# Optimization experiments

Hardware: AMD Instinct MI355X
Metric: run time of the kernel (lower is better)

## Reference

```python
import jax, jax.numpy as jnp
import numpy as np

N = 32768      # nodes
E = 262144     # edges
CS, CV = 32, 16      # node scalar / vector channels (32x0e + 16x1o)
MS, MV = 16, 8       # msg irreps scalar / vector channels
H = 4                # heads
NB = 16              # rbf basis
OS, OV = CS + CV, CS + CV + CV   # CG-coupler output: 48x0e + 64x1o
WNUM = CS + CS + CV + CV + CV    # 112 tensor-product path weights
SPLITS = [CS, CS + CS, CS + CS + CV, CS + CS + CV + CV]
SQRT3, SQRT2 = 3.0 ** 0.5, 2.0 ** 0.5


def _split(x, cs):
    # flat irreps vector -> (scalars [*,cs], vectors [*,cv,3])
    return x[:, :cs], x[:, cs:].reshape(x.shape[0], -1, 3)


def _lin(s, v, Ws, Wv):
    # equivariant o3.Linear: independent mixing of scalar / vector multiplicities
    return s @ Ws, jnp.einsum('ecx,cd->edx', v, Wv)


def _o3_layernorm(s, v, eps=1e-5):
    s = (s - s.mean(-1, keepdims=True)) / jnp.sqrt(s.var(-1, keepdims=True) + eps)
    n2 = jnp.mean(jnp.sum(v * v, -1), -1, keepdims=True)
    return s, v / jnp.sqrt(n2 + eps)[..., None]


def _cg(s, v, y0, y1, w_ss, w_sv, w_vs, w_vd, w_vc):
    # Clebsch-Gordan coupler for l<=1: all allowed paths, per-edge path weights
    dot = jnp.einsum('ecx,ex->ec', v, y1) / SQRT3           # 1o x 1o -> 0e
    cross = jnp.cross(v, y1[:, None, :]) / SQRT2            # 1o x 1o -> 1o
    out_s = jnp.concatenate([w_ss * s * y0[:, None], w_vd * dot], axis=-1)
    out_v = jnp.concatenate([
        w_sv[..., None] * s[..., None] * y1[:, None, :],    # 0e x 1o -> 1o
        w_vs[..., None] * v * y0[:, None, None],            # 1o x 0e -> 1o
        w_vc[..., None] * cross], axis=1)
    return out_s, out_v


def setup_inputs() -> dict:
    key = jax.random.key(0)
    ks = jax.random.split(key, 20)
    w = lambda k, shape, fan: (jax.random.normal(k, shape, jnp.float32) / np.sqrt(fan).astype(np.float32))
    return {
        'node': jax.random.normal(ks[0], (N, CS + 3 * CV), jnp.float32),
        'rbf': jax.random.uniform(ks[1], (E, NB), jnp.float32),
        'rsh': jax.random.normal(ks[2], (E, 4), jnp.float32),
        'Wsrc_s': w(ks[3], (CS, CS), CS), 'Wsrc_v': w(ks[4], (CV, CV), CV),
        'Wdst_s': w(ks[5], (CS, CS), CS), 'Wdst_v': w(ks[6], (CV, CV), CV),
        'W_rbf': w(ks[7], (NB, WNUM), NB),
        'dtp2_w': jax.random.normal(ks[8], (WNUM,), jnp.float32),
        'Wa': w(ks[9], (OS, MS * H), OS),
        'alpha_dot': w(ks[10], (1, H, MS), MS),
        'Wval_s': w(ks[11], (OS, CS), OS), 'Wval_v': w(ks[12], (OV, CV), OV),
        'Wg': w(ks[13], (CS, CV), CS),
        'Wvl_s': w(ks[14], (OS, MS * H), OS), 'Wvl_v': w(ks[15], (OV, MV * H), OV),
        'Wp_s': w(ks[16], (MS * H, CS), MS * H), 'Wp_v': w(ks[17], (MV * H, CV), MV * H),
        'edge_index': jax.random.randint(ks[18], (2, E), 0, N, jnp.int64) if jax.config.read('jax_enable_x64') else jax.random.randint(ks[18], (2, E), 0, N, jnp.int32),
    }


def reference(node, rbf, rsh, Wsrc_s, Wsrc_v, Wdst_s, Wdst_v, W_rbf, dtp2_w, Wa,
              alpha_dot, Wval_s, Wval_v, Wg, Wvl_s, Wvl_v, Wp_s, Wp_v, edge_index):
    src, dst = edge_index[0], edge_index[1]
    y0, y1 = rsh[:, 0], rsh[:, 1:4]

    s, v = _split(node, CS)
    s_n, v_n = _o3_layernorm(s, v)
    ss, sv = _lin(s_n, v_n, Wsrc_s, Wsrc_v)
    ds_, dv = _lin(s_n, v_n, Wdst_s, Wdst_v)
    ms0, mv0 = ss[src] + ds_[dst], sv[src] + dv[dst]          # [E,CS], [E,CV,3]

    w_e = rbf @ W_rbf                                          # per-edge TP weights
    w_ss, w_sv, w_vs, w_vd, w_vc = jnp.split(w_e, SPLITS, axis=-1)
    ms_, mv_ = _cg(ms0, mv0, y0, y1, w_ss, w_sv, w_vs, w_vd, w_vc)  # [E,OS],[E,OV,3]

    # attention scores: leaky_relu + learned dot + edge softmax over dst
    alpha = jax.nn.leaky_relu(ms_ @ Wa, 0.2).reshape(E, H, MS)
    alpha = jnp.sum(alpha * alpha_dot, -1)                     # [E,H]
    m = jax.ops.segment_max(alpha, dst, num_segments=N)
    ea = jnp.exp(alpha - m[dst])
    denom = jax.ops.segment_sum(ea, dst, num_segments=N)
    alpha = ea / denom[dst]

    # value branch: sep_value -> gate -> dtp2 (shared internal weights) -> value_lin
    vs, vv = ms_ @ Wval_s, jnp.einsum('ecx,cd->edx', mv_, Wval_v)
    gv = jax.nn.sigmoid(vs @ Wg)
    vs = vs * jax.nn.sigmoid(vs)
    vv = vv * gv[..., None]
    w2 = jnp.split(dtp2_w[None, :], SPLITS, axis=-1)
    vs2, vv2 = _cg(vs, vv, y0, y1, *w2)
    flat = jnp.concatenate([vs2 @ Wvl_s,
                            jnp.einsum('ecx,cd->edx', vv2, Wvl_v).reshape(E, -1)], -1)
    heads = flat.reshape(E, H, -1)                             # [E,H,(MS+3MV)]

    agg = jax.ops.segment_sum(alpha[..., None] * heads, dst, num_segments=N)
    agg = agg.reshape(N, -1)                                   # [N, MS*H + 3*MV*H]

    fs = agg[:, :MS * H] @ Wp_s
    fv = jnp.einsum('ecx,cd->edx', agg[:, MS * H:].reshape(N, MV * H, 3), Wp_v)
    feat = jnp.concatenate([fs, fv.reshape(N, -1)], -1)
    return node + feat
```

## Files before the change

### kernel.cpp

```cpp
#include <hip/hip_runtime.h>

#define NN 32768
#define EE 262144

static __device__ __forceinline__ float sigm(float x){
  return 1.0f / (1.0f + __expf(-x));
}

__global__ __launch_bounds__(256) void k_node(
    const float* __restrict__ node,
    const float* __restrict__ Wss, const float* __restrict__ Wsv,
    const float* __restrict__ Wds, const float* __restrict__ Wdv,
    float* __restrict__ ss, float* __restrict__ ds,
    float* __restrict__ sv, float* __restrict__ dv)
{
  int n = blockIdx.x * 256 + threadIdx.x;
  if (n >= NN) return;
  const float4* row = reinterpret_cast<const float4*>(node + (size_t)n * 80);
  float s[32], v[48];
#pragma unroll
  for (int i = 0; i < 8; ++i){
    float4 t = row[i];
    s[i*4+0]=t.x; s[i*4+1]=t.y; s[i*4+2]=t.z; s[i*4+3]=t.w;
  }
#pragma unroll
  for (int i = 0; i < 12; ++i){
    float4 t = row[8+i];
    v[i*4+0]=t.x; v[i*4+1]=t.y; v[i*4+2]=t.z; v[i*4+3]=t.w;
  }
  float mean = 0.f;
#pragma unroll
  for (int i=0;i<32;++i) mean += s[i];
  mean *= (1.0f/32.0f);
  float var = 0.f;
#pragma unroll
  for (int i=0;i<32;++i){ float d0 = s[i]-mean; var += d0*d0; }
  var *= (1.0f/32.0f);
  float sinv = rsqrtf(var + 1e-5f);
#pragma unroll
  for (int i=0;i<32;++i) s[i] = (s[i]-mean)*sinv;
  float n2 = 0.f;
#pragma unroll
  for (int i=0;i<48;++i) n2 += v[i]*v[i];
  n2 *= (1.0f/16.0f);
  float vinv = rsqrtf(n2 + 1e-5f);
#pragma unroll
  for (int i=0;i<48;++i) v[i] *= vinv;

  float* ssr = ss + (size_t)n*32;
  float* dsr = ds + (size_t)n*32;
#pragma unroll 1
  for (int d=0; d<32; ++d){
    float a=0.f, b=0.f;
#pragma unroll
    for (int c=0;c<32;++c){ a += s[c]*Wss[c*32+d]; b += s[c]*Wds[c*32+d]; }
    ssr[d]=a; dsr[d]=b;
  }
  float* svr = sv + (size_t)n*48;
  float* dvr = dv + (size_t)n*48;
#pragma unroll 1
  for (int d=0; d<16; ++d){
#pragma unroll
    for (int x=0;x<3;++x){
      float a=0.f, b=0.f;
#pragma unroll
      for (int c=0;c<16;++c){ a += v[c*3+x]*Wsv[c*16+d]; b += v[c*3+x]*Wdv[c*16+d]; }
      svr[d*3+x]=a; dvr[d*3+x]=b;
    }
  }
}

__global__ __launch_bounds__(256) void k_hist(const int* __restrict__ ei, int* __restrict__ deg){
  int e = blockIdx.x*256 + threadIdx.x;
  if (e >= EE) return;
  atomicAdd(deg + ei[EE + e], 1);
}

__global__ __launch_bounds__(1024) void k_scan(const int* __restrict__ deg,
                                               int* __restrict__ base, int* __restrict__ cursor){
  __shared__ int lds[1024];
  int t = threadIdx.x;
  int v[32];
#pragma unroll
  for (int i=0;i<32;++i) v[i] = deg[t*32+i];
  int run = 0;
#pragma unroll
  for (int i=0;i<32;++i){ int x=v[i]; v[i]=run; run+=x; }
  lds[t]=run; __syncthreads();
  for (int off=1; off<1024; off<<=1){
    int add = (t>=off) ? lds[t-off] : 0;
    __syncthreads();
    lds[t] += add;
    __syncthreads();
  }
  int pre = (t==0) ? 0 : lds[t-1];
#pragma unroll
  for (int i=0;i<32;++i){ int b = pre + v[i]; base[t*32+i]=b; cursor[t*32+i]=b; }
}

__global__ __launch_bounds__(256) void k_scatter(const int* __restrict__ ei,
                                                 int* __restrict__ cursor, int* __restrict__ csr){
  int e = blockIdx.x*256 + threadIdx.x;
  if (e >= EE) return;
  int d = ei[EE + e];
  int pos = atomicAdd(cursor + d, 1);
  csr[pos] = e;
}

#define A_RBFA 0
#define A_RBFD 640
#define A_WA   960
#define A_ADOT 4288
#define A_EDG  4352
#define A_ESTR 152

__global__ __launch_bounds__(512) void k_edgeA2(
    const int* __restrict__ ei,
    const float* __restrict__ rbf, const float* __restrict__ rsh,
    const float* __restrict__ Wrbf, const float* __restrict__ Wa,
    const float* __restrict__ adot,
    const float* __restrict__ ss, const float* __restrict__ ds,
    const float* __restrict__ sv, const float* __restrict__ dv,
    float* __restrict__ logits)
{
  __shared__ __align__(16) float SH[A_EDG + 16*A_ESTR];
  const int t = threadIdx.x;
  for (int i=t; i<32*16; i+=512){ int row=i>>4, j=i&15; SH[A_RBFA+row*20+j] = Wrbf[j*112+row]; }
  for (int i=t; i<16*16; i+=512){ int row=i>>4, j=i&15; SH[A_RBFD+row*20+j] = Wrbf[j*112+80+row]; }
  for (int i=t; i<64*48; i+=512){ int o=i/48, k=i-48*o; SH[A_WA+o*52+k] = Wa[k*64+o]; }
  for (int i=t; i<64;    i+=512){ SH[A_ADOT+i] = adot[i]; }
  __syncthreads();

  const int g = t >> 5;
  const int c = t & 31;
  float* E = &SH[A_EDG + g*A_ESTR];
  const float IS3 = 0.57735026918962576f;

#pragma unroll 1
  for (int tile=0; tile<16; ++tile){
    const int e = blockIdx.x*256 + tile*16 + g;
    const int src = ei[e], dst = ei[EE + e];

    if (c < 8){
      float4 a = *reinterpret_cast<const float4*>(ss + (size_t)src*32 + c*4);
      float4 b = *reinterpret_cast<const float4*>(ds + (size_t)dst*32 + c*4);
      float4 o; o.x=a.x+b.x; o.y=a.y+b.y; o.z=a.z+b.z; o.w=a.w+b.w;
      *reinterpret_cast<float4*>(&E[c*4]) = o;
    } else if (c < 20){
      int i = c-8;
      float4 a = *reinterpret_cast<const float4*>(sv + (size_t)src*48 + i*4);
      float4 b = *reinterpret_cast<const float4*>(dv + (size_t)dst*48 + i*4);
      float4 o; o.x=a.x+b.x; o.y=a.y+b.y; o.z=a.z+b.z; o.w=a.w+b.w;
      *reinterpret_cast<float4*>(&E[32+i*4]) = o;
    } else if (c < 24){
      int i = c-20;
      *reinterpret_cast<float4*>(&E[80+i*4]) =
          *reinterpret_cast<const float4*>(rbf + (size_t)e*16 + i*4);
    } else if (c == 24){
      *reinterpret_cast<float4*>(&E[96]) =
          *reinterpret_cast<const float4*>(rsh + (size_t)e*4);
    }

    float rr[16];
#pragma unroll
    for (int i=0;i<4;++i) *reinterpret_cast<float4*>(&rr[i*4]) =
        *reinterpret_cast<const float4*>(&E[80+i*4]);
    const float y0=E[96], y1x=E[97], y1y=E[98], y1z=E[99];
    {
      float wA=0.f;
#pragma unroll
      for (int j4=0;j4<4;++j4){
        float4 a0 = *reinterpret_cast<const float4*>(&SH[A_RBFA + c*20 + j4*4]);
        wA += rr[j4*4+0]*a0.x + rr[j4*4+1]*a0.y + rr[j4*4+2]*a0.z + rr[j4*4+3]*a0.w;
      }
      E[104+c] = wA * E[c] * y0;
    }
    if (c < 16){
      float wD=0.f;
#pragma unroll
      for (int j4=0;j4<4;++j4){
        float4 a0 = *reinterpret_cast<const float4*>(&SH[A_RBFD + c*20 + j4*4]);
        wD += rr[j4*4+0]*a0.x + rr[j4*4+1]*a0.y + rr[j4*4+2]*a0.z + rr[j4*4+3]*a0.w;
      }
      float vx=E[32+c*3], vy=E[33+c*3], vz=E[34+c*3];
      E[136+c] = wD * (vx*y1x + vy*y1y + vz*y1z) * IS3;
    }

    float mm[48];
#pragma unroll
    for (int k4=0;k4<12;++k4) *reinterpret_cast<float4*>(&mm[k4*4]) =
        *reinterpret_cast<const float4*>(&E[104+k4*4]);
    float acc0=0.f, acc1=0.f;
#pragma unroll
    for (int k4=0;k4<12;++k4){
      float4 w0 = *reinterpret_cast<const float4*>(&SH[A_WA + c*52 + k4*4]);
      float4 w1 = *reinterpret_cast<const float4*>(&SH[A_WA + (32+c)*52 + k4*4]);
      acc0 += mm[k4*4+0]*w0.x + mm[k4*4+1]*w0.y + mm[k4*4+2]*w0.z + mm[k4*4+3]*w0.w;
      acc1 += mm[k4*4+0]*w1.x + mm[k4*4+1]*w1.y + mm[k4*4+2]*w1.z + mm[k4*4+3]*w1.w;
    }
    acc0 = ((acc0 > 0.f) ? acc0 : 0.2f*acc0) * SH[A_ADOT+c];
    acc1 = ((acc1 > 0.f) ? acc1 : 0.2f*acc1) * SH[A_ADOT+32+c];
#pragma unroll
    for (int msk=8; msk>=1; msk>>=1){
      acc0 += __shfl_xor(acc0, msk);
      acc1 += __shfl_xor(acc1, msk);
    }
    if ((c & 15) == 0){
      int h0 = c >> 4;
      logits[(size_t)e*4 + h0]     = acc0;
      logits[(size_t)e*4 + 2 + h0] = acc1;
    }
  }
}

__global__ __launch_bounds__(256) void k_soft(
    const int* __restrict__ base, const int* __restrict__ deg,
    const int* __restrict__ csr, const float* __restrict__ logits,
    float* __restrict__ m, float* __restrict__ iden)
{
  int id = blockIdx.x*256 + threadIdx.x;
  if (id >= NN*4) return;
  int d = id >> 2, h = id & 3;
  int b = base[d], n = deg[d];
  float mm = -3.4e38f;
  for (int i=0;i<n;++i){ int e = csr[b+i]; mm = fmaxf(mm, logits[(size_t)e*4+h]); }
  float s = 0.f;
  for (int i=0;i<n;++i){ int e = csr[b+i]; s += __expf(logits[(size_t)e*4+h] - mm); }
  m[id] = mm;
  iden[id] = (n>0) ? 1.0f/s : 0.f;
}

#define CA_RBF  0
#define CA_VALS 2240
#define CA_VVA  3904
#define CA_VVB  4480
#define CA_VVC  4800
#define CA_G    5120
#define CA_EDG  5696
#define CA_ESTR 400

__global__ __launch_bounds__(256) void k_edgeCa(
    const int* __restrict__ csr, const int* __restrict__ ei,
    const float* __restrict__ rbf, const float* __restrict__ rsh,
    const float* __restrict__ Wrbf,
    const float* __restrict__ Wvals, const float* __restrict__ Wvalv,
    const float* __restrict__ Wg,
    const float* __restrict__ ss, const float* __restrict__ ds,
    const float* __restrict__ sv, const float* __restrict__ dv,
    const float* __restrict__ logits, const float* __restrict__ m,
    const float* __restrict__ iden, float* __restrict__ wflat)
{
  __shared__ __align__(16) float SH[CA_EDG + 8*CA_ESTR];
  const int t = threadIdx.x;
  for (int i=t; i<112*16; i+=256){ int d=i>>4, k=i&15; SH[CA_RBF+d*20+k]  = Wrbf[k*112+d]; }
  for (int i=t; i<32*48;  i+=256){ int d=i/48, k=i-48*d; SH[CA_VALS+d*52+k] = Wvals[k*32+d]; }
  for (int i=t; i<16*32;  i+=256){ int d=i>>5, k=i&31; SH[CA_VVA+d*36+k]  = Wvalv[k*16+d]; }
  for (int i=t; i<16*16;  i+=256){ int d=i>>4, k=i&15; SH[CA_VVB+d*20+k]  = Wvalv[(32+k)*16+d]; }
  for (int i=t; i<16*16;  i+=256){ int d=i>>4, k=i&15; SH[CA_VVC+d*20+k]  = Wvalv[(48+k)*16+d]; }
  for (int i=t; i<16*32;  i+=256){ int d=i>>5, k=i&31; SH[CA_G+d*36+k]    = Wg[k*16+d]; }
  __syncthreads();

  const int g = t >> 5;
  const int c = t & 31;
  float* E = &SH[CA_EDG + g*CA_ESTR];
  const float IS3 = 0.57735026918962576f;
  const float IS2 = 0.70710678118654752f;

#pragma unroll 1
  for (int tile=0; tile<16; ++tile){
    const int pidx = blockIdx.x*128 + tile*8 + g;
    const int e = csr[pidx];
    const int src = ei[e], dst = ei[EE + e];

    if (c < 8){
      float4 a = *reinterpret_cast<const float4*>(ss + (size_t)src*32 + c*4);
      float4 b = *reinterpret_cast<const float4*>(ds + (size_t)dst*32 + c*4);
      float4 o; o.x=a.x+b.x; o.y=a.y+b.y; o.z=a.z+b.z; o.w=a.w+b.w;
      *reinterpret_cast<float4*>(&E[c*4]) = o;
    } else if (c < 20){
      int i = c-8;
      float4 a = *reinterpret_cast<const float4*>(sv + (size_t)src*48 + i*4);
      float4 b = *reinterpret_cast<const float4*>(dv + (size_t)dst*48 + i*4);
      float4 o; o.x=a.x+b.x; o.y=a.y+b.y; o.z=a.z+b.z; o.w=a.w+b.w;
      *reinterpret_cast<float4*>(&E[32+i*4]) = o;
    } else if (c < 24){
      int i = c-20;
      *reinterpret_cast<float4*>(&E[80+i*4]) =
          *reinterpret_cast<const float4*>(rbf + (size_t)e*16 + i*4);
    } else if (c == 24){
      *reinterpret_cast<float4*>(&E[96]) =
          *reinterpret_cast<const float4*>(rsh + (size_t)e*4);
    } else if (c == 25){
      float4 l4 = *reinterpret_cast<const float4*>(logits + (size_t)e*4);
      float4 m4 = *reinterpret_cast<const float4*>(m + (size_t)dst*4);
      float4 i4 = *reinterpret_cast<const float4*>(iden + (size_t)dst*4);
      E[100] = __expf(l4.x-m4.x)*i4.x;
      E[101] = __expf(l4.y-m4.y)*i4.y;
      E[102] = __expf(l4.z-m4.z)*i4.z;
      E[103] = __expf(l4.w-m4.w)*i4.w;
    }

    float rr[16];
#pragma unroll
    for (int i=0;i<4;++i) *reinterpret_cast<float4*>(&rr[i*4]) =
        *reinterpret_cast<const float4*>(&E[80+i*4]);
    float wA=0.f, wB=0.f, wC=0.f, wD=0.f;
#pragma unroll
    for (int j4=0;j4<4;++j4){
      float4 a0 = *reinterpret_cast<const float4*>(&SH[CA_RBF + c*20           + j4*4]);
      float4 a1 = *reinterpret_cast<const float4*>(&SH[CA_RBF + (32+c)*20      + j4*4]);
      float4 a2 = *reinterpret_cast<const float4*>(&SH[CA_RBF + (64+c)*20      + j4*4]);
      float4 a3 = *reinterpret_cast<const float4*>(&SH[CA_RBF + (96+(c&15))*20 + j4*4]);
      float r0=rr[j4*4+0], r1=rr[j4*4+1], r2=rr[j4*4+2], r3=rr[j4*4+3];
      wA += r0*a0.x + r1*a0.y + r2*a0.z + r3*a0.w;
      wB += r0*a1.x + r1*a1.y + r2*a1.z + r3*a1.w;
      wC += r0*a2.x + r1*a2.y + r2*a2.z + r3*a2.w;
      wD += r0*a3.x + r1*a3.y + r2*a3.z + r3*a3.w;
    }

    const float y0=E[96], y1x=E[97], y1y=E[98], y1z=E[99];
    const float s_c = E[c];
    E[104+c] = wA * s_c * y0;
    E[152+c] = wB * s_c;
    if (c >= 16){
      int k = c-16;
      float vx=E[32+k*3], vy=E[33+k*3], vz=E[34+k*3];
      E[136+k] = wC * (vx*y1x+vy*y1y+vz*y1z) * IS3;
    }
    if (c < 16){
      int k = c;
      float vx=E[32+k*3], vy=E[33+k*3], vz=E[34+k*3];
      float u = wC * y0;
      E[200+k]    = u*vx; E[216+k] = u*vy; E[232+k] = u*vz;
      float cx=(vy*y1z - vz*y1y)*IS2;
      float cy=(vz*y1x - vx*y1z)*IS2;
      float cz=(vx*y1y - vy*y1x)*IS2;
      E[248+k]    = wD*cx; E[264+k] = wD*cy; E[280+k] = wD*cz;
    }

    if (c < 16){
      float acc=0.f, accB=0.f;
#pragma unroll
      for (int k4=0;k4<8;k4+=2){
        float4 w0 = *reinterpret_cast<const float4*>(&SH[CA_VVA + c*36 + k4*4]);
        float4 t0 = *reinterpret_cast<const float4*>(&E[152+k4*4]);
        float4 w1 = *reinterpret_cast<const float4*>(&SH[CA_VVA + c*36 + k4*4+4]);
        float4 t1 = *reinterpret_cast<const float4*>(&E[152+k4*4+4]);
        acc  += w0.x*t0.x + w0.y*t0.y + w0.z*t0.z + w0.w*t0.w;
        accB += w1.x*t1.x + w1.y*t1.y + w1.z*t1.z + w1.w*t1.w;
      }
      E[184+c]=acc+accB;
    }

    {
      int d0=c/3, x0=c-3*d0;
      float acc0 = E[184+d0]*E[97+x0];
#pragma unroll
      for (int k4=0;k4<4;++k4){
        float4 wb = *reinterpret_cast<const float4*>(&SH[CA_VVB + d0*20 + k4*4]);
        float4 wc = *reinterpret_cast<const float4*>(&SH[CA_VVC + d0*20 + k4*4]);
        float4 pp = *reinterpret_cast<const float4*>(&E[200 + x0*16 + k4*4]);
        float4 qq = *reinterpret_cast<const float4*>(&E[248 + x0*16 + k4*4]);
        acc0 += pp.x*wb.x+pp.y*wb.y+pp.z*wb.z+pp.w*wb.w
              + qq.x*wc.x+qq.y*wc.y+qq.z*wc.z+qq.w*wc.w;
      }
      E[344+c]=acc0;
      if (c < 16){
        int l=32+c, d1=l/3, x1=l-3*d1;
        float acc1 = E[184+d1]*E[97+x1];
#pragma unroll
        for (int k4=0;k4<4;++k4){
          float4 wb = *reinterpret_cast<const float4*>(&SH[CA_VVB + d1*20 + k4*4]);
          float4 wc = *reinterpret_cast<const float4*>(&SH[CA_VVC + d1*20 + k4*4]);
          float4 pp = *reinterpret_cast<const float4*>(&E[200 + x1*16 + k4*4]);
          float4 qq = *reinterpret_cast<const float4*>(&E[248 + x1*16 + k4*4]);
          acc1 += pp.x*wb.x+pp.y*wb.y+pp.z*wb.z+pp.w*wb.w
                + qq.x*wc.x+qq.y*wc.y+qq.z*wc.z+qq.w*wc.w;
        }
        E[344+l]=acc1;
      }
    }

    float accv=0.f, accw=0.f;
#pragma unroll
    for (int k4=0;k4<12;k4+=2){
      float4 w0 = *reinterpret_cast<const float4*>(&SH[CA_VALS + c*52 + k4*4]);
      float4 m0 = *reinterpret_cast<const float4*>(&E[104+k4*4]);
      float4 w1 = *reinterpret_cast<const float4*>(&SH[CA_VALS + c*52 + k4*4+4]);
      float4 m1 = *reinterpret_cast<const float4*>(&E[104+k4*4+4]);
      accv += w0.x*m0.x + w0.y*m0.y + w0.z*m0.z + w0.w*m0.w;
      accw += w1.x*m1.x + w1.y*m1.y + w1.z*m1.z + w1.w*m1.w;
    }
    accv += accw;
    E[296+c]=accv;

    if (c < 16){
      float acc=0.f;
#pragma unroll
      for (int k4=0;k4<8;++k4){
        float4 ww = *reinterpret_cast<const float4*>(&SH[CA_G + c*36 + k4*4]);
        float4 vv4 = *reinterpret_cast<const float4*>(&E[296+k4*4]);
        acc += ww.x*vv4.x + ww.y*vv4.y + ww.z*vv4.z + ww.w*vv4.w;
      }
      E[328+c]=sigm(acc);
    }

    float* erow = wflat + (size_t)pidx*160;
    erow[c] = accv * sigm(accv);
    erow[32+c] = E[344+c]*E[328+c/3];
    if (c < 16){
      int l = 32+c;
      erow[64+c] = E[344+l]*E[328+l/3];
    }
    if (c < 8){
      erow[80+c] = (c<4) ? E[100+c] : E[96+c-4];
    }
  }
}

#define CB_VLS  0
#define CB_VLVA 3328
#define CB_VLVB 4480
#define CB_VLVC 5120
#define CB_W2   5760
#define CB_EDG  5872
#define CB_ESTR 240

__global__ __launch_bounds__(256) void k_edgeCb(
    const float* __restrict__ Wvls, const float* __restrict__ Wvlv,
    const float* __restrict__ w2, float* __restrict__ wflat)
{
  __shared__ __align__(16) float SH[CB_EDG + 8*CB_ESTR];
  const int t = threadIdx.x;
  for (int i=t; i<64*48; i+=256){ int d=i/48, k=i-48*d; SH[CB_VLS+d*52+k] = Wvls[k*64+d]; }
  for (int i=t; i<32*32; i+=256){ int d=i>>5, k=i&31; SH[CB_VLVA+d*36+k] = Wvlv[k*32+d]; }
  for (int i=t; i<32*16; i+=256){ int d=i>>4, k=i&15; SH[CB_VLVB+d*20+k] = Wvlv[(32+k)*32+d]; }
  for (int i=t; i<32*16; i+=256){ int d=i>>4, k=i&15; SH[CB_VLVC+d*20+k] = Wvlv[(48+k)*32+d]; }
  for (int i=t; i<112;   i+=256){ SH[CB_W2+i] = w2[i]; }
  __syncthreads();

  const int g = t >> 5;
  const int c = t & 31;
  float* E = &SH[CB_EDG + g*CB_ESTR];
  const float IS3 = 0.57735026918962576f;
  const float IS2 = 0.70710678118654752f;

#pragma unroll 1
  for (int tile=0; tile<16; ++tile){
    const int pidx = blockIdx.x*128 + tile*8 + g;
    float* wrow = wflat + (size_t)pidx*160;

    const float vsc = wrow[c];
    E[c] = wrow[32+c];
    if (c < 16) E[32+c] = wrow[64+c];
    if (c < 8)  E[48+c] = wrow[80+c];

    const float y0=E[52], y1x=E[53], y1y=E[54], y1z=E[55];

    E[104+c] = SH[CB_W2+32+c]*vsc;
    E[56+c]  = SH[CB_W2+c]*vsc*y0;
    if (c >= 16){
      int k = c-16;
      float gx=E[k*3], gy=E[k*3+1], gz=E[k*3+2];
      E[88+k] = SH[CB_W2+80+k]*(gx*y1x+gy*y1y+gz*y1z)*IS3;
    }
    if (c < 16){
      int k = c;
      float gx=E[k*3], gy=E[k*3+1], gz=E[k*3+2];
      float u = SH[CB_W2+64+k]*y0;
      E[136+k]=u*gx; E[152+k]=u*gy; E[168+k]=u*gz;
      float cx=(gy*y1z - gz*y1y)*IS2;
      float cy=(gz*y1x - gx*y1z)*IS2;
      float cz=(gx*y1y - gy*y1x)*IS2;
      float wq = SH[CB_W2+96+k];
      E[184+k]=wq*cx; E[200+k]=wq*cy; E[216+k]=wq*cz;
    }

    const float a0=E[48], a1=E[49], a2h=E[50], a3h=E[51];

    {
      float f0a=0.f, f0b=0.f, f1a=0.f, f1b=0.f;
#pragma unroll
      for (int k4=0;k4<12;k4+=2){
        float4 v0 = *reinterpret_cast<const float4*>(&E[56+k4*4]);
        float4 v1 = *reinterpret_cast<const float4*>(&E[56+k4*4+4]);
        float4 wa0 = *reinterpret_cast<const float4*>(&SH[CB_VLS + c*52 + k4*4]);
        float4 wa1 = *reinterpret_cast<const float4*>(&SH[CB_VLS + c*52 + k4*4+4]);
        float4 wb0 = *reinterpret_cast<const float4*>(&SH[CB_VLS + (32+c)*52 + k4*4]);
        float4 wb1 = *reinterpret_cast<const float4*>(&SH[CB_VLS + (32+c)*52 + k4*4+4]);
        f0a += v0.x*wa0.x + v0.y*wa0.y + v0.z*wa0.z + v0.w*wa0.w;
        f0b += v1.x*wa1.x + v1.y*wa1.y + v1.z*wa1.z + v1.w*wa1.w;
        f1a += v0.x*wb0.x + v0.y*wb0.y + v0.z*wb0.z + v0.w*wb0.w;
        f1b += v1.x*wb1.x + v1.y*wb1.y + v1.z*wb1.z + v1.w*wb1.w;
      }
      wrow[c]    = (f0a+f0b)*a0;
      wrow[32+c] = (f1a+f1b)*((c<8)?a0:a1);
    }

    {
      float A2=0.f, A2b=0.f;
#pragma unroll
      for (int k4=0;k4<8;k4+=2){
        float4 w0 = *reinterpret_cast<const float4*>(&SH[CB_VLVA + c*36 + k4*4]);
        float4 t0 = *reinterpret_cast<const float4*>(&E[104+k4*4]);
        float4 w1 = *reinterpret_cast<const float4*>(&SH[CB_VLVA + c*36 + k4*4+4]);
        float4 t1 = *reinterpret_cast<const float4*>(&E[104+k4*4+4]);
        A2  += w0.x*t0.x + w0.y*t0.y + w0.z*t0.z + w0.w*t0.w;
        A2b += w1.x*t1.x + w1.y*t1.y + w1.z*t1.z + w1.w*t1.w;
      }
      A2 += A2b;
      float b0=A2*y1x, b1=A2*y1y, b2=A2*y1z;
#pragma unroll
      for (int k4=0;k4<4;++k4){
        float4 wb = *reinterpret_cast<const float4*>(&SH[CB_VLVB + c*20 + k4*4]);
        float4 wc = *reinterpret_cast<const float4*>(&SH[CB_VLVC + c*20 + k4*4]);
        float4 p0 = *reinterpret_cast<const float4*>(&E[136 + k4*4]);
        float4 p1 = *reinterpret_cast<const float4*>(&E[152 + k4*4]);
        float4 p2v= *reinterpret_cast<const float4*>(&E[168 + k4*4]);
        float4 q0 = *reinterpret_cast<const float4*>(&E[184 + k4*4]);
        float4 q1 = *reinterpret_cast<const float4*>(&E[200 + k4*4]);
        float4 q2v= *reinterpret_cast<const float4*>(&E[216 + k4*4]);
        b0 += p0.x*wb.x+p0.y*wb.y+p0.z*wb.z+p0.w*wb.w + q0.x*wc.x+q0.y*wc.y+q0.z*wc.z+q0.w*wc.w;
        b1 += p1.x*wb.x+p1.y*wb.y+p1.z*wb.z+p1.w*wb.w + q1.x*wc.x+q1.y*wc.y+q1.z*wc.z+q1.w*wc.w;
        b2 += p2v.x*wb.x+p2v.y*wb.y+p2v.z*wb.z+p2v.w*wb.w + q2v.x*wc.x+q2v.y*wc.y+q2v.z*wc.z+q2v.w*wc.w;
      }
      int o = 64 + c*3;
      float aw0 = (o   < 80) ? a1 : ((o   < 120) ? a2h : a3h);
      float aw1 = (o+1 < 80) ? a1 : ((o+1 < 120) ? a2h : a3h);
      float aw2 = (o+2 < 80) ? a1 : ((o+2 < 120) ? a2h : a3h);
      wrow[o]   = b0*aw0;
      wrow[o+1] = b1*aw1;
      wrow[o+2] = b2*aw2;
    }
  }
}

__global__ __launch_bounds__(256) void k_gather(
    const int* __restrict__ base, const int* __restrict__ deg,
    const float* __restrict__ wflat, float* __restrict__ agg)
{
  int id = blockIdx.x*256 + threadIdx.x;
  if (id >= NN*40) return;
  int d = id / 40, c = id % 40;
  int b = base[d], n = deg[d];
  float4 acc = make_float4(0.f,0.f,0.f,0.f);
  for (int i=0;i<n;++i){
    float4 w = reinterpret_cast<const float4*>(wflat + (size_t)(b+i)*160)[c];
    acc.x += w.x; acc.y += w.y; acc.z += w.z; acc.w += w.w;
  }
  reinterpret_cast<float4*>(agg + (size_t)d*160)[c] = acc;
}

__global__ __launch_bounds__(256) void k_out(
    const float* __restrict__ node, const float* __restrict__ agg,
    const float* __restrict__ Wps, const float* __restrict__ Wpv,
    float* __restrict__ out)
{
  int n = blockIdx.x * 256 + threadIdx.x;
  if (n >= NN) return;
  const float* ar = agg + (size_t)n*160;
  const float* nr = node + (size_t)n*80;
  float* orow = out + (size_t)n*80;

  float a[64];
  { const float4* ap = reinterpret_cast<const float4*>(ar);
#pragma unroll
    for (int i=0;i<16;++i){ float4 t=ap[i];
      a[i*4]=t.x; a[i*4+1]=t.y; a[i*4+2]=t.z; a[i*4+3]=t.w; } }
#pragma unroll 1
  for (int d=0; d<32; ++d){
    float acc=0.f;
#pragma unroll
    for (int c=0;c<64;++c) acc += a[c]*Wps[c*32+d];
    orow[d] = nr[d] + acc;
  }
  float b[96];
  { const float4* bp = reinterpret_cast<const float4*>(ar + 64);
#pragma unroll
    for (int i=0;i<24;++i){ float4 t=bp[i];
      b[i*4]=t.x; b[i*4+1]=t.y; b[i*4+2]=t.z; b[i*4+3]=t.w; } }
#pragma unroll 1
  for (int d=0; d<16; ++d){
#pragma unroll
    for (int x=0;x<3;++x){
      float acc=0.f;
#pragma unroll
      for (int c=0;c<32;++c) acc += b[c*3+x]*Wpv[c*16+d];
      orow[32+d*3+x] = nr[32+d*3+x] + acc;
    }
  }
}

extern "C" void kernel_launch(void* const* d_in, const int* in_sizes, int n_in,
                              void* d_out, int out_size, void* d_ws, size_t ws_size,
                              hipStream_t stream)
{
  const float* node   = (const float*)d_in[0];
  const float* rbf    = (const float*)d_in[1];
  const float* rsh    = (const float*)d_in[2];
  const float* Wsrc_s = (const float*)d_in[3];
  const float* Wsrc_v = (const float*)d_in[4];
  const float* Wdst_s = (const float*)d_in[5];
  const float* Wdst_v = (const float*)d_in[6];
  const float* W_rbf  = (const float*)d_in[7];
  const float* dtp2   = (const float*)d_in[8];
  const float* Wa     = (const float*)d_in[9];
  const float* adot   = (const float*)d_in[10];
  const float* Wval_s = (const float*)d_in[11];
  const float* Wval_v = (const float*)d_in[12];
  const float* Wg     = (const float*)d_in[13];
  const float* Wvl_s  = (const float*)d_in[14];
  const float* Wvl_v  = (const float*)d_in[15];
  const float* Wp_s   = (const float*)d_in[16];
  const float* Wp_v   = (const float*)d_in[17];
  const int*   ei     = (const int*)d_in[18];

  float* ws = (float*)d_ws;

  size_t off = 0;
  float* ss   = ws + off; off += (size_t)NN*32;
  float* ds   = ws + off; off += (size_t)NN*32;
  float* sv   = ws + off; off += (size_t)NN*48;
  float* dv   = ws + off; off += (size_t)NN*48;
  float* lg   = ws + off; off += (size_t)EE*4;
  float* m    = ws + off; off += (size_t)NN*4;
  float* iden = ws + off; off += (size_t)NN*4;
  int* deg    = (int*)(ws + off); off += (size_t)NN;
  int* base   = (int*)(ws + off); off += (size_t)NN;
  int* cursor = (int*)(ws + off); off += (size_t)NN;
  int* csr    = (int*)(ws + off); off += (size_t)EE;
  float* agg  = ws + off; off += (size_t)NN*160;
  float* wflat= ws + off; off += (size_t)EE*160;
  size_t need_new = off * sizeof(float);
  if (ws_size < need_new) return;

  hipMemsetAsync(deg, 0, (size_t)NN*sizeof(int), stream);
  k_node   <<<NN/256, 256, 0, stream>>>(node, Wsrc_s, Wsrc_v, Wdst_s, Wdst_v, ss, ds, sv, dv);
  k_hist   <<<EE/256, 256, 0, stream>>>(ei, deg);
  k_scan   <<<1, 1024, 0, stream>>>(deg, base, cursor);
  k_scatter<<<EE/256, 256, 0, stream>>>(ei, cursor, csr);
  k_edgeA2 <<<EE/256, 512, 0, stream>>>(ei, rbf, rsh, W_rbf, Wa, adot, ss, ds, sv, dv, lg);
  k_soft   <<<(NN*4)/256, 256, 0, stream>>>(base, deg, csr, lg, m, iden);
  k_edgeCa <<<EE/128, 256, 0, stream>>>(csr, ei, rbf, rsh, W_rbf, Wval_s, Wval_v, Wg,
                                        ss, ds, sv, dv, lg, m, iden, wflat);
  k_edgeCb <<<EE/128, 256, 0, stream>>>(Wvl_s, Wvl_v, dtp2, wflat);
  k_gather <<<(NN*40)/256, 256, 0, stream>>>(base, deg, wflat, agg);
  k_out    <<<NN/256, 256, 0, stream>>>(node, agg, Wp_s, Wp_v, (float*)d_out);
}
```

Baseline: 577.5 us.

## Fuse per-destination aggregation into edge value kernel with segmented atomics

The edge value kernel now walks CSR-sorted edges in contiguous runs per warp group, accumulates outputs in registers while the destination stays the same, and flushes them to the aggregate buffer with atomic adds when it changes. This removes the separate gather kernel and the full 160-float per-edge write/read round trip, and shrinks the intermediate per-edge buffer from 160 to 96 floats. In exchange it adds a sorted destination array, a memset of the aggregate buffer and float atomics whose ordering makes results nondeterministic.

```diff
diff --git a/kernel.cpp b/kernel.cpp
--- a/kernel.cpp
+++ b/kernel.cpp
@@ -99,12 +99,14 @@
 }
 
 __global__ __launch_bounds__(256) void k_scatter(const int* __restrict__ ei,
-                                                 int* __restrict__ cursor, int* __restrict__ csr){
+                                                 int* __restrict__ cursor, int* __restrict__ csr,
+                                                 int* __restrict__ dsts){
   int e = blockIdx.x*256 + threadIdx.x;
   if (e >= EE) return;
   int d = ei[EE + e];
   int pos = atomicAdd(cursor + d, 1);
   csr[pos] = e;
+  dsts[pos] = d;
 }
 
 #define A_RBFA 0
@@ -405,7 +407,7 @@
       E[328+c]=sigm(acc);
     }
 
-    float* erow = wflat + (size_t)pidx*160;
+    float* erow = wflat + (size_t)pidx*96;
     erow[c] = accv * sigm(accv);
     erow[32+c] = E[344+c]*E[328+c/3];
     if (c < 16){
@@ -427,8 +429,10 @@
 #define CB_ESTR 240
 
 __global__ __launch_bounds__(256) void k_edgeCb(
+    const int* __restrict__ dsts,
     const float* __restrict__ Wvls, const float* __restrict__ Wvlv,
-    const float* __restrict__ w2, float* __restrict__ wflat)
+    const float* __restrict__ w2, const float* __restrict__ wflat,
+    float* __restrict__ agg)
 {
   __shared__ __align__(16) float SH[CB_EDG + 8*CB_ESTR];
   const int t = threadIdx.x;
@@ -445,10 +449,25 @@
   const float IS3 = 0.57735026918962576f;
   const float IS2 = 0.70710678118654752f;
 
+  const int p0 = blockIdx.x*128 + g*16;
+  int cur = dsts[p0];
+  float ac0=0.f, ac1=0.f, ac2=0.f, ac3=0.f, ac4=0.f;
+
 #pragma unroll 1
   for (int tile=0; tile<16; ++tile){
-    const int pidx = blockIdx.x*128 + tile*8 + g;
-    float* wrow = wflat + (size_t)pidx*160;
+    const int pidx = p0 + tile;
+    const int dst = dsts[pidx];
+    if (dst != cur){
+      float* ar = agg + (size_t)cur*160;
+      atomicAdd(ar+c,       ac0);
+      atomicAdd(ar+32+c,    ac1);
+      atomicAdd(ar+64+c*3,  ac2);
+      atomicAdd(ar+65+c*3,  ac3);
+      atomicAdd(ar+66+c*3,  ac4);
+      ac0=ac1=ac2=ac3=ac4=0.f;
+      cur = dst;
+    }
+    const float* wrow = wflat + (size_t)pidx*96;
 
     const float vsc = wrow[c];
     E[c] = wrow[32+c];
@@ -493,8 +512,8 @@
         f1a += v0.x*wb0.x + v0.y*wb0.y + v0.z*wb0.z + v0.w*wb0.w;
         f1b += v1.x*wb1.x + v1.y*wb1.y + v1.z*wb1.z + v1.w*wb1.w;
       }
-      wrow[c]    = (f0a+f0b)*a0;
-      wrow[32+c] = (f1a+f1b)*((c<8)?a0:a1);
+      ac0 += (f0a+f0b)*a0;
+      ac1 += (f1a+f1b)*((c<8)?a0:a1);
     }
 
     {
@@ -514,41 +533,34 @@
       for (int k4=0;k4<4;++k4){
         float4 wb = *reinterpret_cast<const float4*>(&SH[CB_VLVB + c*20 + k4*4]);
         float4 wc = *reinterpret_cast<const float4*>(&SH[CB_VLVC + c*20 + k4*4]);
-        float4 p0 = *reinterpret_cast<const float4*>(&E[136 + k4*4]);
-        float4 p1 = *reinterpret_cast<const float4*>(&E[152 + k4*4]);
-        float4 p2v= *reinterpret_cast<const float4*>(&E[168 + k4*4]);
-        float4 q0 = *reinterpret_cast<const float4*>(&E[184 + k4*4]);
-        float4 q1 = *reinterpret_cast<const float4*>(&E[200 + k4*4]);
-        float4 q2v= *reinterpret_cast<const float4*>(&E[216 + k4*4]);
-        b0 += p0.x*wb.x+p0.y*wb.y+p0.z*wb.z+p0.w*wb.w + q0.x*wc.x+q0.y*wc.y+q0.z*wc.z+q0.w*wc.w;
-        b1 += p1.x*wb.x+p1.y*wb.y+p1.z*wb.z+p1.w*wb.w + q1.x*wc.x+q1.y*wc.y+q1.z*wc.z+q1.w*wc.w;
-        b2 += p2v.x*wb.x+p2v.y*wb.y+p2v.z*wb.z+p2v.w*wb.w + q2v.x*wc.x+q2v.y*wc.y+q2v.z*wc.z+q2v.w*wc.w;
+        float4 pp0 = *reinterpret_cast<const float4*>(&E[136 + k4*4]);
+        float4 pp1 = *reinterpret_cast<const float4*>(&E[152 + k4*4]);
+        float4 pp2 = *reinterpret_cast<const float4*>(&E[168 + k4*4]);
+        float4 qq0 = *reinterpret_cast<const float4*>(&E[184 + k4*4]);
+        float4 qq1 = *reinterpret_cast<const float4*>(&E[200 + k4*4]);
+        float4 qq2 = *reinterpret_cast<const float4*>(&E[216 + k4*4]);
+        b0 += pp0.x*wb.x+pp0.y*wb.y+pp0.z*wb.z+pp0.w*wb.w + qq0.x*wc.x+qq0.y*wc.y+qq0.z*wc.z+qq0.w*wc.w;
+        b1 += pp1.x*wb.x+pp1.y*wb.y+pp1.z*wb.z+pp1.w*wb.w + qq1.x*wc.x+qq1.y*wc.y+qq1.z*wc.z+qq1.w*wc.w;
+        b2 += pp2.x*wb.x+pp2.y*wb.y+pp2.z*wb.z+pp2.w*wb.w + qq2.x*wc.x+qq2.y*wc.y+qq2.z*wc.z+qq2.w*wc.w;
       }
       int o = 64 + c*3;
       float aw0 = (o   < 80) ? a1 : ((o   < 120) ? a2h : a3h);
       float aw1 = (o+1 < 80) ? a1 : ((o+1 < 120) ? a2h : a3h);
       float aw2 = (o+2 < 80) ? a1 : ((o+2 < 120) ? a2h : a3h);
-      wrow[o]   = b0*aw0;
-      wrow[o+1] = b1*aw1;
-      wrow[o+2] = b2*aw2;
-    }
-  }
-}
-
-__global__ __launch_bounds__(256) void k_gather(
-    const int* __restrict__ base, const int* __restrict__ deg,
-    const float* __restrict__ wflat, float* __restrict__ agg)
-{
-  int id = blockIdx.x*256 + threadIdx.x;
-  if (id >= NN*40) return;
-  int d = id / 40, c = id % 40;
-  int b = base[d], n = deg[d];
-  float4 acc = make_float4(0.f,0.f,0.f,0.f);
-  for (int i=0;i<n;++i){
-    float4 w = reinterpret_cast<const float4*>(wflat + (size_t)(b+i)*160)[c];
-    acc.x += w.x; acc.y += w.y; acc.z += w.z; acc.w += w.w;
-  }
-  reinterpret_cast<float4*>(agg + (size_t)d*160)[c] = acc;
+      ac2 += b0*aw0;
+      ac3 += b1*aw1;
+      ac4 += b2*aw2;
+    }
+  }
+
+  {
+    float* ar = agg + (size_t)cur*160;
+    atomicAdd(ar+c,       ac0);
+    atomicAdd(ar+32+c,    ac1);
+    atomicAdd(ar+64+c*3,  ac2);
+    atomicAdd(ar+65+c*3,  ac3);
+    atomicAdd(ar+66+c*3,  ac4);
+  }
 }
 
 __global__ __launch_bounds__(256) void k_out(
@@ -629,21 +641,22 @@
   int* base   = (int*)(ws + off); off += (size_t)NN;
   int* cursor = (int*)(ws + off); off += (size_t)NN;
   int* csr    = (int*)(ws + off); off += (size_t)EE;
+  int* dsts   = (int*)(ws + off); off += (size_t)EE;
   float* agg  = ws + off; off += (size_t)NN*160;
-  float* wflat= ws + off; off += (size_t)EE*160;
+  float* wflat= ws + off; off += (size_t)EE*96;
   size_t need_new = off * sizeof(float);
   if (ws_size < need_new) return;
 
   hipMemsetAsync(deg, 0, (size_t)NN*sizeof(int), stream);
+  hipMemsetAsync(agg, 0, (size_t)NN*160*sizeof(float), stream);
   k_node   <<<NN/256, 256, 0, stream>>>(node, Wsrc_s, Wsrc_v, Wdst_s, Wdst_v, ss, ds, sv, dv);
   k_hist   <<<EE/256, 256, 0, stream>>>(ei, deg);
   k_scan   <<<1, 1024, 0, stream>>>(deg, base, cursor);
-  k_scatter<<<EE/256, 256, 0, stream>>>(ei, cursor, csr);
+  k_scatter<<<EE/256, 256, 0, stream>>>(ei, cursor, csr, dsts);
   k_edgeA2 <<<EE/256, 512, 0, stream>>>(ei, rbf, rsh, W_rbf, Wa, adot, ss, ds, sv, dv, lg);
   k_soft   <<<(NN*4)/256, 256, 0, stream>>>(base, deg, csr, lg, m, iden);
   k_edgeCa <<<EE/128, 256, 0, stream>>>(csr, ei, rbf, rsh, W_rbf, Wval_s, Wval_v, Wg,
                                         ss, ds, sv, dv, lg, m, iden, wflat);
-  k_edgeCb <<<EE/128, 256, 0, stream>>>(Wvl_s, Wvl_v, dtp2, wflat);
-  k_gather <<<(NN*40)/256, 256, 0, stream>>>(base, deg, wflat, agg);
+  k_edgeCb <<<EE/128, 256, 0, stream>>>(dsts, Wvl_s, Wvl_v, dtp2, wflat, agg);
   k_out    <<<NN/256, 256, 0, stream>>>(node, agg, Wp_s, Wp_v, (float*)d_out);
 }
```

New measurement: 639.1 us. 1.11x slower.
